# Optimization experiments

Measured on AMD Instinct MI355X. Metric: run time of the kernel, lower is better.

## Reference

```python
import jax, jax.numpy as jnp
import numpy as np

GRID = 16
K = 2
NW = (GRID - K + 1) ** 2  # 225 sliding 2x2 windows on the 16x16 grid


def _make_mask():
    idx = np.arange(GRID * GRID).reshape(GRID, GRID)
    wins = np.stack([idx[i:i + K, j:j + K].ravel()
                     for i in range(GRID - K + 1) for j in range(GRID - K + 1)])
    m = np.zeros((NW, GRID * GRID), np.float32)
    m[np.arange(NW)[:, None], wins] = 1.0
    return jnp.asarray(m)

MASK = _make_mask()          # [225, 256] window -> covered cells
MASK_COUNT = MASK.sum(0)     # windows covering each cell
BN_SCALE = np.float32(1.0 / np.sqrt(1.0 + 1e-5))  # eval BN, running mean=0 var=1


def _adapter(x, w1, w2):
    return jax.nn.relu(jax.nn.relu(x @ w1.T) @ w2.T)


def _bn(x, g, b):
    return x * (g * BN_SCALE) + b


def _head(x, w1, b1, g2, be2, w2, b2, g3, be3, w3, b3):
    x = _bn(jax.nn.relu(x @ w1.T + b1), g2, be2)
    x = _bn(jax.nn.relu(x @ w2.T + b2), g3, be3)
    return jax.nn.sigmoid(x @ w3.T + b3)[:, 0]


def setup_inputs() -> dict:
    B, L, P, D, R, S = 64, 3, 225, 640, 1800, 240
    key = jax.random.key(0)
    ks = jax.random.split(key, 16)
    n = lambda k, s, sc=1.0: jax.random.normal(k, s, jnp.float32) * sc
    te = n(ks[3], (2, D)); te = te / jnp.linalg.norm(te, axis=-1, keepdims=True)
    pr = n(ks[5], (L, R, D)); pr = pr / jnp.linalg.norm(pr, axis=-1, keepdims=True)
    w = 0.05
    return dict(
        image=n(ks[0], (B, 3, S, S)),
        image_embeds=n(ks[1], (B, D)),
        patch_embeds=n(ks[2], (L, B, P, D)),
        text_embeds=te,
        image_embeds_ref=n(ks[4], (1, D)),
        patch_embeds_ref=pr,
        a_w1=n(ks[6], (160, D), w), a_w2=n(ks[7], (D, 160), w),
        r_w1=n(ks[8], (128, D), w), r_b1=jnp.zeros((128,)),
        r_g2=jnp.ones((128,)), r_be2=jnp.zeros((128,)),
        r_w2=n(ks[9], (64, 128), w), r_b2=jnp.zeros((64,)),
        r_g3=jnp.ones((64,)), r_be3=jnp.zeros((64,)),
        r_w3=n(ks[10], (1, 64), w), r_b3=jnp.zeros((1,)),
        h_w1=n(ks[11], (128, P), w), h_b1=jnp.zeros((128,)),
        h_g2=jnp.ones((128,)), h_be2=jnp.zeros((128,)),
        h_w2=n(ks[12], (64, 128), w), h_b2=jnp.zeros((64,)),
        h_g3=jnp.ones((64,)), h_be3=jnp.zeros((64,)),
        h_w3=n(ks[13], (1, 64), w), h_b3=jnp.zeros((1,)),
    )


def reference(image, image_embeds, patch_embeds, text_embeds, image_embeds_ref,
              patch_embeds_ref, a_w1, a_w2,
              r_w1, r_b1, r_g2, r_be2, r_w2, r_b2, r_g3, r_be3, r_w3, r_b3,
              h_w1, h_b1, h_g2, h_be2, h_w2, h_b2, h_g3, h_be3, h_w3, h_b3):
    pe = patch_embeds / jnp.linalg.norm(patch_embeds, axis=-1, keepdims=True)
    nie = image_embeds / jnp.linalg.norm(image_embeds, axis=-1, keepdims=True)
    text_score = jax.nn.softmax(100.0 * nie @ text_embeds.T, axis=-1)[:, 1]
    # kNN-style min-distance over reference patches: [L,B,P,R]
    sim = jnp.einsum('lbpd,lrd->lbpr', pe, patch_embeds_ref)
    patch_ref_map = ((1.0 - sim).min(axis=3) / 2.0).mean(axis=0)  # [B,P]
    fg_score = patch_ref_map.max(axis=1)
    diff = image_embeds_ref - _adapter(image_embeds, a_w1, a_w2)
    img_ref_score = _head(diff, r_w1, r_b1, r_g2, r_be2, r_w2, r_b2, r_g3, r_be3, r_w3, r_b3)
    holistic = (text_score + img_ref_score)[:, None] + patch_ref_map  # [B,225]
    hl_score = _head(holistic, h_w1, h_b1, h_g2, h_be2, h_w2, h_b2, h_g3, h_be3, h_w3, h_b3)
    final_score = (hl_score + fg_score) / 2.0
    # harmonic aggregation of window scores onto the 16x16 grid
    heat = (MASK_COUNT / ((1.0 / holistic) @ MASK)).reshape(-1, GRID, GRID)
    hmap = jax.image.resize(heat, (heat.shape[0], image.shape[2], image.shape[3]), 'bilinear')
    return final_score, hmap
```

## Files before the change

kernel.cpp:

```cpp
#include <hip/hip_runtime.h>
#include <stdint.h>
#include <math.h>

#define L_DIM 3
#define B_DIM 64
#define P_DIM 225
#define D_DIM 640
#define R_DIM 1800
#define S_DIM 240
#define M_TOT 14400
#define M_PAD 14592
#define N_PAD 2048
#define MT 57
#define NT 8
#define KT 10
#define BNSCALE 0.99999500003749981f

typedef __bf16 bf16x8 __attribute__((ext_vector_type(8)));
typedef float f32x4 __attribute__((ext_vector_type(4)));

__device__ __forceinline__ unsigned short f2bf(float f) {
    union { float f; unsigned u; } v; v.f = f;
    unsigned u = v.u;
    unsigned r = (u + 0x7FFFu + ((u >> 16) & 1u)) >> 16;
    return (unsigned short)r;
}

__global__ __launch_bounds__(256)
void k_convert(const float* __restrict__ pe, const float* __restrict__ per,
               unsigned short* __restrict__ abf, unsigned short* __restrict__ rbf,
               float* __restrict__ rnorm)
{
    const int AROWS = L_DIM * M_PAD;
    int wid = (blockIdx.x * 256 + threadIdx.x) >> 6;
    int lane = threadIdx.x & 63;
    const ushort4 z4 = {0, 0, 0, 0};
    if (wid < AROWS) {
        int l = wid / M_PAD, r = wid - l * M_PAD;
        unsigned short* dst = abf + (size_t)wid * D_DIM;
        if (r < M_TOT) {
            const float4* src = (const float4*)(pe + ((size_t)l * M_TOT + r) * D_DIM);
            float ss = 0.f;
            #pragma unroll
            for (int it = 0; it < 3; ++it) {
                int idx = it * 64 + lane;
                if (idx < 160) {
                    float4 v = src[idx];
                    ss += v.x * v.x + v.y * v.y + v.z * v.z + v.w * v.w;
                    ushort4 o;
                    o.x = f2bf(v.x); o.y = f2bf(v.y); o.z = f2bf(v.z); o.w = f2bf(v.w);
                    *(ushort4*)(dst + idx * 4) = o;
                }
            }
            #pragma unroll
            for (int m = 32; m; m >>= 1) ss += __shfl_xor(ss, m);
            if (lane == 0) rnorm[l * M_TOT + r] = rsqrtf(ss);
        } else {
            #pragma unroll
            for (int it = 0; it < 3; ++it) {
                int idx = it * 64 + lane;
                if (idx < 160) *(ushort4*)(dst + idx * 4) = z4;
            }
        }
    } else {
        int w2 = wid - AROWS;
        int l = w2 / N_PAD, r = w2 - l * N_PAD;
        unsigned short* dst = rbf + (size_t)w2 * D_DIM;
        if (r < R_DIM) {
            const float4* src = (const float4*)(per + ((size_t)l * R_DIM + r) * D_DIM);
            #pragma unroll
            for (int it = 0; it < 3; ++it) {
                int idx = it * 64 + lane;
                if (idx < 160) {
                    float4 v = src[idx];
                    ushort4 o;
                    o.x = f2bf(v.x); o.y = f2bf(v.y); o.z = f2bf(v.z); o.w = f2bf(v.w);
                    *(ushort4*)(dst + idx * 4) = o;
                }
            }
        } else {
            #pragma unroll
            for (int it = 0; it < 3; ++it) {
                int idx = it * 64 + lane;
                if (idx < 160) *(ushort4*)(dst + idx * 4) = z4;
            }
        }
    }
}

#define MFMA(A, B, C) __builtin_amdgcn_mfma_f32_16x16x32_bf16((A), (B), (C), 0, 0, 0)
#define GLL(SRC, DSTOFF)                                                     \
    __builtin_amdgcn_global_load_lds(                                        \
        (const __attribute__((address_space(1))) void*)(SRC),               \
        (__attribute__((address_space(3))) void*)(lds + (DSTOFF)), 16, 0, 0)

#define PHASE_TAIL(NJB, STG0, STG1, VMSTR)                                   \
    {                                                                        \
        bf16x8 b00 = *(const bf16x8*)(lds + bB + (brow0 + (NJB) * 16) * 64 + sw0);     \
        bf16x8 b01 = *(const bf16x8*)(lds + bB + (brow0 + (NJB) * 16) * 64 + sw1);     \
        bf16x8 b10 = *(const bf16x8*)(lds + bB + (brow0 + (NJB + 1) * 16) * 64 + sw0); \
        bf16x8 b11 = *(const bf16x8*)(lds + bB + (brow0 + (NJB + 1) * 16) * 64 + sw1); \
        STG0; STG1;                                                          \
        asm volatile("s_waitcnt " VMSTR ::: "memory");                       \
        __builtin_amdgcn_s_barrier();                                        \
        __builtin_amdgcn_s_setprio(1);                                       \
        _Pragma("unroll")                                                    \
        for (int mi = 0; mi < 4; ++mi) {                                     \
            acc[mi][NJB]     = MFMA(a[mi][0], b00, acc[mi][NJB]);            \
            acc[mi][NJB]     = MFMA(a[mi][1], b01, acc[mi][NJB]);            \
            acc[mi][NJB + 1] = MFMA(a[mi][0], b10, acc[mi][NJB + 1]);        \
            acc[mi][NJB + 1] = MFMA(a[mi][1], b11, acc[mi][NJB + 1]);        \
        }                                                                    \
        __builtin_amdgcn_s_setprio(0);                                       \
    }

__global__ __launch_bounds__(512, 2)
void k_gemm_max(const unsigned short* __restrict__ abf,
                const unsigned short* __restrict__ rbf,
                float* __restrict__ pmax)
{
    __shared__ unsigned short lds[65536];
    __shared__ float red[2][256];

    int bid = blockIdx.x;
    int v = (bid & 7) * 171 + (bid >> 3);
    int l = v / (MT * NT);
    int rem = v - l * (MT * NT);
    int mt = rem >> 3;
    int nt = rem & 7;

    int tid = threadIdx.x;
    int wid = tid >> 6, lane = tid & 63;
    int wm = wid >> 1;
    int wn = wid & 1;
    int lane15 = lane & 15, lg = lane >> 4;
    int sA = lane15 & 7;
    int sw0 = ((lg) ^ sA) << 3;
    int sw1 = ((4 + lg) ^ sA) << 3;
    int arow0 = wm * 64 + lane15;
    int brow0 = wn * 128 + lane15;

    int rowc = lane >> 3;
    int scol = ((lane & 7) ^ rowc) << 3;
    const unsigned short* gA = abf + (size_t)(l * M_PAD + mt * 256) * D_DIM;
    const unsigned short* gB = rbf + (size_t)(l * N_PAD + nt * 256) * D_DIM;
    int chA0 = wid, chA1 = 8 + wid, chA2 = 16 + wid, chA3 = 24 + wid;
    int chB0 = (wid < 4) ? (0 + wid) : (12 + wid);
    int chB1 = (wid < 4) ? (4 + wid) : (16 + wid);
    int chB2 = (wid < 4) ? (8 + wid) : (20 + wid);
    int chB3 = (wid < 4) ? (12 + wid) : (24 + wid);
    const unsigned short* pA0 = gA + (size_t)(chA0 * 8 + rowc) * D_DIM + scol;
    const unsigned short* pA1 = gA + (size_t)(chA1 * 8 + rowc) * D_DIM + scol;
    const unsigned short* pA2 = gA + (size_t)(chA2 * 8 + rowc) * D_DIM + scol;
    const unsigned short* pA3 = gA + (size_t)(chA3 * 8 + rowc) * D_DIM + scol;
    const unsigned short* pB0 = gB + (size_t)(chB0 * 8 + rowc) * D_DIM + scol;
    const unsigned short* pB1 = gB + (size_t)(chB1 * 8 + rowc) * D_DIM + scol;
    const unsigned short* pB2 = gB + (size_t)(chB2 * 8 + rowc) * D_DIM + scol;
    const unsigned short* pB3 = gB + (size_t)(chB3 * 8 + rowc) * D_DIM + scol;

    f32x4 acc[4][8];
    #pragma unroll
    for (int mi = 0; mi < 4; ++mi)
        #pragma unroll
        for (int nj = 0; nj < 8; ++nj)
            acc[mi][nj] = f32x4{0.f, 0.f, 0.f, 0.f};

    GLL(pA0, chA0 * 512); GLL(pA1, chA1 * 512);
    GLL(pA2, chA2 * 512); GLL(pA3, chA3 * 512);
    GLL(pB0, 32768 + chB0 * 512); GLL(pB1, 32768 + chB1 * 512);
    GLL(pB2, 32768 + chB2 * 512); GLL(pB3, 32768 + chB3 * 512);
    asm volatile("s_waitcnt vmcnt(3)" ::: "memory");
    __builtin_amdgcn_s_barrier();

    int buf = 0;
    for (int kt = 0; kt < KT; ++kt) {
        int ob = buf ^ 1;
        int aB = buf * 16384;
        int bB = 32768 + buf * 16384;
        int oaB = ob * 16384;
        int obB = 32768 + ob * 16384;
        int koff = (kt + 1 < KT ? kt + 1 : KT - 1) * 64;

        bf16x8 a[4][2];
        #pragma unroll
        for (int mi = 0; mi < 4; ++mi) {
            a[mi][0] = *(const bf16x8*)(lds + aB + (arow0 + mi * 16) * 64 + sw0);
            a[mi][1] = *(const bf16x8*)(lds + aB + (arow0 + mi * 16) * 64 + sw1);
        }
        PHASE_TAIL(0, GLL(pA0 + koff, oaB + chA0 * 512),
                      GLL(pA1 + koff, oaB + chA1 * 512), "vmcnt(4)")
        PHASE_TAIL(2, GLL(pA2 + koff, oaB + chA2 * 512),
                      GLL(pA3 + koff, oaB + chA3 * 512), "vmcnt(5)")
        PHASE_TAIL(4, GLL(pB0 + koff, obB + chB0 * 512),
                      GLL(pB1 + koff, obB + chB1 * 512), "vmcnt(6)")
        PHASE_TAIL(6, GLL(pB2 + koff, obB + chB2 * 512),
                      GLL(pB3 + koff, obB + chB3 * 512), "vmcnt(3)")
        buf = ob;
    }

    __syncthreads();

    int colbase = nt * 256 + wn * 128 + lane15;
    #pragma unroll
    for (int mi = 0; mi < 4; ++mi) {
        float t[4] = {-__builtin_inff(), -__builtin_inff(),
                      -__builtin_inff(), -__builtin_inff()};
        #pragma unroll
        for (int nj = 0; nj < 8; ++nj) {
            if (colbase + nj * 16 < R_DIM) {
                #pragma unroll
                for (int r = 0; r < 4; ++r) t[r] = fmaxf(t[r], acc[mi][nj][r]);
            }
        }
        #pragma unroll
        for (int m = 1; m <= 8; m <<= 1) {
            #pragma unroll
            for (int r = 0; r < 4; ++r) t[r] = fmaxf(t[r], __shfl_xor(t[r], m));
        }
        if (lane15 == 0) {
            int rb = wm * 64 + mi * 16 + lg * 4;
            #pragma unroll
            for (int r = 0; r < 4; ++r) red[wn][rb + r] = t[r];
        }
    }
    __syncthreads();
    if (tid < 256) {
        float vmx = fmaxf(red[0][tid], red[1][tid]);
        pmax[((size_t)l * NT + nt) * M_PAD + mt * 256 + tid] = vmx;
    }
}

__global__ __launch_bounds__(256)
void k_combine(const float* __restrict__ pmax, const float* __restrict__ rnorm,
               float* __restrict__ prm)
{
    int r = blockIdx.x * 256 + threadIdx.x;
    if (r >= M_TOT) return;
    float s = 0.f;
    #pragma unroll
    for (int l = 0; l < L_DIM; ++l) {
        float m = -__builtin_inff();
        #pragma unroll
        for (int t = 0; t < NT; ++t)
            m = fmaxf(m, pmax[((size_t)l * NT + t) * M_PAD + r]);
        s += m * rnorm[l * M_TOT + r];
    }
    prm[r] = (3.0f - s) / 6.0f;
}

__device__ __forceinline__ float block_sum8(float v, volatile float* scratch) {
    #pragma unroll
    for (int m = 32; m; m >>= 1) v += __shfl_xor(v, m);
    int w = threadIdx.x >> 6;
    __syncthreads();
    if ((threadIdx.x & 63) == 0) scratch[w] = v;
    __syncthreads();
    float r = 0.f;
    #pragma unroll
    for (int i = 0; i < 8; ++i) r += scratch[i];
    return r;
}
__device__ __forceinline__ float block_max8(float v, volatile float* scratch) {
    #pragma unroll
    for (int m = 32; m; m >>= 1) v = fmaxf(v, __shfl_xor(v, m));
    int w = threadIdx.x >> 6;
    __syncthreads();
    if ((threadIdx.x & 63) == 0) scratch[w] = v;
    __syncthreads();
    float r = scratch[0];
    #pragma unroll
    for (int i = 1; i < 8; ++i) r = fmaxf(r, scratch[i]);
    return r;
}

__global__ __launch_bounds__(512)
void k_small(const float* __restrict__ ie, const float* __restrict__ te,
             const float* __restrict__ ier,
             const float* __restrict__ a_w1, const float* __restrict__ a_w2,
             const float* __restrict__ r_w1, const float* __restrict__ r_b1,
             const float* __restrict__ r_g2, const float* __restrict__ r_be2,
             const float* __restrict__ r_w2, const float* __restrict__ r_b2,
             const float* __restrict__ r_g3, const float* __restrict__ r_be3,
             const float* __restrict__ r_w3, const float* __restrict__ r_b3,
             const float* __restrict__ h_w1, const float* __restrict__ h_b1,
             const float* __restrict__ h_g2, const float* __restrict__ h_be2,
             const float* __restrict__ h_w2, const float* __restrict__ h_b2,
             const float* __restrict__ h_g3, const float* __restrict__ h_be3,
             const float* __restrict__ h_w3, const float* __restrict__ h_b3,
             const float* __restrict__ prm, float* __restrict__ heat,
             float* __restrict__ out_score)
{
    int b = blockIdx.x, tid = threadIdx.x;
    __shared__ float x[D_DIM];
    __shared__ float h1[160];
    __shared__ float dif[D_DIM];
    __shared__ float z1[128];
    __shared__ float z2[64];
    __shared__ float hol[P_DIM];
    __shared__ float rcp[P_DIM];
    __shared__ float scratch[8];

    for (int i = tid; i < D_DIM; i += 512) x[i] = ie[b * D_DIM + i];
    __syncthreads();

    float ss = 0.f, d0 = 0.f, d1 = 0.f;
    for (int i = tid; i < D_DIM; i += 512) {
        float v = x[i];
        ss += v * v;
        d0 += v * te[i];
        d1 += v * te[D_DIM + i];
    }
    float ssum = block_sum8(ss, scratch);
    float dd0 = block_sum8(d0, scratch);
    float dd1 = block_sum8(d1, scratch);
    float tscore = 1.f / (1.f + expf(100.f * rsqrtf(ssum) * (dd0 - dd1)));

    for (int o = tid; o < 160; o += 512) {
        const float* w = a_w1 + (size_t)o * D_DIM;
        float s0 = 0, s1 = 0, s2 = 0, s3 = 0;
        for (int d = 0; d < D_DIM; d += 4) {
            s0 += x[d] * w[d]; s1 += x[d + 1] * w[d + 1];
            s2 += x[d + 2] * w[d + 2]; s3 += x[d + 3] * w[d + 3];
        }
        h1[o] = fmaxf((s0 + s1) + (s2 + s3), 0.f);
    }
    __syncthreads();
    for (int d = tid; d < D_DIM; d += 512) {
        const float* w = a_w2 + (size_t)d * 160;
        float s0 = 0, s1 = 0, s2 = 0, s3 = 0;
        for (int o = 0; o < 160; o += 4) {
            s0 += h1[o] * w[o]; s1 += h1[o + 1] * w[o + 1];
            s2 += h1[o + 2] * w[o + 2]; s3 += h1[o + 3] * w[o + 3];
        }
        dif[d] = ier[d] - fmaxf((s0 + s1) + (s2 + s3), 0.f);
    }
    __syncthreads();

    for (int o = tid; o < 128; o += 512) {
        const float* w = r_w1 + (size_t)o * D_DIM;
        float s0 = 0, s1 = 0, s2 = 0, s3 = 0;
        for (int d = 0; d < D_DIM; d += 4) {
            s0 += dif[d] * w[d]; s1 += dif[d + 1] * w[d + 1];
            s2 += dif[d + 2] * w[d + 2]; s3 += dif[d + 3] * w[d + 3];
        }
        float s = (s0 + s1) + (s2 + s3) + r_b1[o];
        z1[o] = fmaxf(s, 0.f) * (r_g2[o] * BNSCALE) + r_be2[o];
    }
    __syncthreads();
    for (int o = tid; o < 64; o += 512) {
        const float* w = r_w2 + (size_t)o * 128;
        float s = r_b2[o];
        for (int d = 0; d < 128; ++d) s += z1[d] * w[d];
        z2[o] = fmaxf(s, 0.f) * (r_g3[o] * BNSCALE) + r_be3[o];
    }
    __syncthreads();
    float sp = (tid < 64) ? z2[tid] * r_w3[tid] : 0.f;
    float irs = 1.f / (1.f + expf(-(block_sum8(sp, scratch) + r_b3[0])));

    float fgp = -__builtin_inff();
    float base = tscore + irs;
    for (int p = tid; p < P_DIM; p += 512) {
        float pv = prm[b * P_DIM + p];
        fgp = fmaxf(fgp, pv);
        float h = base + pv;
        hol[p] = h;
        rcp[p] = 1.f / h;
    }
    float fg = block_max8(fgp, scratch);

    for (int o = tid; o < 128; o += 512) {
        const float* w = h_w1 + (size_t)o * P_DIM;
        float s = h_b1[o];
        for (int d = 0; d < P_DIM; ++d) s += hol[d] * w[d];
        z1[o] = fmaxf(s, 0.f) * (h_g2[o] * BNSCALE) + h_be2[o];
    }
    __syncthreads();
    for (int o = tid; o < 64; o += 512) {
        const float* w = h_w2 + (size_t)o * 128;
        float s = h_b2[o];
        for (int d = 0; d < 128; ++d) s += z1[d] * w[d];
        z2[o] = fmaxf(s, 0.f) * (h_g3[o] * BNSCALE) + h_be3[o];
    }
    __syncthreads();
    float sp2 = (tid < 64) ? z2[tid] * h_w3[tid] : 0.f;
    float hl_in = block_sum8(sp2, scratch) + h_b3[0];
    if (tid == 0) {
        float hl = 1.f / (1.f + expf(-hl_in));
        out_score[b] = (hl + fg) * 0.5f;
    }

    if (tid < 256) {
        int r = tid >> 4, c = tid & 15;
        float s = 0.f, cnt = 0.f;
        #pragma unroll
        for (int di = -1; di <= 0; ++di) {
            int i = r + di;
            if (i < 0 || i > 14) continue;
            #pragma unroll
            for (int dj = -1; dj <= 0; ++dj) {
                int j = c + dj;
                if (j < 0 || j > 14) continue;
                s += rcp[i * 15 + j];
                cnt += 1.f;
            }
        }
        heat[b * 256 + tid] = cnt / s;
    }
}

__global__ __launch_bounds__(256)
void k_resize(const float* __restrict__ heat, float* __restrict__ outh)
{
    int b = blockIdx.x >> 3, sub = blockIdx.x & 7;
    __shared__ float h[256];
    if (threadIdx.x < 256) h[threadIdx.x] = heat[b * 256 + threadIdx.x];
    __syncthreads();
    int base = sub * 30 * S_DIM;
    for (int q = threadIdx.x; q < 30 * S_DIM; q += 256) {
        int px = base + q;
        int y = px / S_DIM, xc = px - y * S_DIM;
        float sy = fminf(fmaxf((y - 7) * (1.0f / 15.0f), 0.f), 15.f);
        float sx = fminf(fmaxf((xc - 7) * (1.0f / 15.0f), 0.f), 15.f);
        int y0 = (int)sy, x0 = (int)sx;
        int y1 = min(y0 + 1, 15), x1 = min(x0 + 1, 15);
        float fy = sy - (float)y0, fx = sx - (float)x0;
        float v00 = h[y0 * 16 + x0], v01 = h[y0 * 16 + x1];
        float v10 = h[y1 * 16 + x0], v11 = h[y1 * 16 + x1];
        float v = (1.f - fy) * ((1.f - fx) * v00 + fx * v01)
                + fy * ((1.f - fx) * v10 + fx * v11);
        outh[(size_t)b * (S_DIM * S_DIM) + px] = v;
    }
}

extern "C" void kernel_launch(void* const* d_in, const int* in_sizes, int n_in,
                              void* d_out, int out_size, void* d_ws, size_t ws_size,
                              hipStream_t stream)
{
    (void)in_sizes; (void)n_in; (void)out_size; (void)ws_size;
    const float* image_embeds = (const float*)d_in[1];
    const float* patch_embeds = (const float*)d_in[2];
    const float* text_embeds  = (const float*)d_in[3];
    const float* ier          = (const float*)d_in[4];
    const float* per          = (const float*)d_in[5];
    const float* a_w1 = (const float*)d_in[6];
    const float* a_w2 = (const float*)d_in[7];
    const float* r_w1 = (const float*)d_in[8];
    const float* r_b1 = (const float*)d_in[9];
    const float* r_g2 = (const float*)d_in[10];
    const float* r_be2 = (const float*)d_in[11];
    const float* r_w2 = (const float*)d_in[12];
    const float* r_b2 = (const float*)d_in[13];
    const float* r_g3 = (const float*)d_in[14];
    const float* r_be3 = (const float*)d_in[15];
    const float* r_w3 = (const float*)d_in[16];
    const float* r_b3 = (const float*)d_in[17];
    const float* h_w1 = (const float*)d_in[18];
    const float* h_b1 = (const float*)d_in[19];
    const float* h_g2 = (const float*)d_in[20];
    const float* h_be2 = (const float*)d_in[21];
    const float* h_w2 = (const float*)d_in[22];
    const float* h_b2 = (const float*)d_in[23];
    const float* h_g3 = (const float*)d_in[24];
    const float* h_be3 = (const float*)d_in[25];
    const float* h_w3 = (const float*)d_in[26];
    const float* h_b3 = (const float*)d_in[27];

    char* ws = (char*)d_ws;
    size_t off = 0;
    auto take = [&](size_t bytes) -> void* {
        void* p = ws + off;
        off += (bytes + 255) & ~(size_t)255;
        return p;
    };
    float* rnorm = (float*)take((size_t)L_DIM * M_TOT * 4);
    float* pmax  = (float*)take((size_t)L_DIM * NT * M_PAD * 4);
    float* prm   = (float*)take((size_t)M_TOT * 4);
    float* heat  = (float*)take((size_t)B_DIM * 256 * 4);
    unsigned short* abf = (unsigned short*)take((size_t)L_DIM * M_PAD * D_DIM * 2);
    unsigned short* rbf = (unsigned short*)take((size_t)L_DIM * N_PAD * D_DIM * 2);

    float* out_f = (float*)d_out;

    k_convert<<<dim3((L_DIM * M_PAD + L_DIM * N_PAD) / 4), dim3(256), 0, stream>>>(
        patch_embeds, per, abf, rbf, rnorm);
    k_gemm_max<<<dim3(L_DIM * MT * NT), dim3(512), 0, stream>>>(abf, rbf, pmax);
    k_combine<<<dim3((M_TOT + 255) / 256), dim3(256), 0, stream>>>(pmax, rnorm, prm);
    k_small<<<dim3(B_DIM), dim3(512), 0, stream>>>(image_embeds, text_embeds, ier,
        a_w1, a_w2, r_w1, r_b1, r_g2, r_be2, r_w2, r_b2, r_g3, r_be3, r_w3, r_b3,
        h_w1, h_b1, h_g2, h_be2, h_w2, h_b2, h_g3, h_be3, h_w3, h_b3,
        prm, heat, out_f);
    k_resize<<<dim3(B_DIM * 8), dim3(256), 0, stream>>>(heat, out_f + B_DIM);
}
```

Measured before the change: 204.5 us.

## Software-pipeline LDS fragment reads in GEMM and fuse combine into small kernel

The GEMM inner loop now prefetches the next B-quarter and the next k-tile's A/B fragments into registers before issuing the current MFMAs, ping-ponging between two register sets. The goal is to hide LDS read latency behind MFMA work instead of stalling after each barrier. The separate k_combine kernel is removed and its max/normalize reduction is folded into k_small, which saves one launch and a round trip through global memory. In exchange the prefetch buffers raise register pressure at launch_bounds(512,2), and k_small's per-block work grows slightly.

```diff
diff --git a/kernel.cpp b/kernel.cpp
--- a/kernel.cpp
+++ b/kernel.cpp
@@ -94,25 +94,26 @@
         (const __attribute__((address_space(1))) void*)(SRC),               \
         (__attribute__((address_space(3))) void*)(lds + (DSTOFF)), 16, 0, 0)
 
-#define PHASE_TAIL(NJB, STG0, STG1, VMSTR)                                   \
-    {                                                                        \
-        bf16x8 b00 = *(const bf16x8*)(lds + bB + (brow0 + (NJB) * 16) * 64 + sw0);     \
-        bf16x8 b01 = *(const bf16x8*)(lds + bB + (brow0 + (NJB) * 16) * 64 + sw1);     \
-        bf16x8 b10 = *(const bf16x8*)(lds + bB + (brow0 + (NJB + 1) * 16) * 64 + sw0); \
-        bf16x8 b11 = *(const bf16x8*)(lds + bB + (brow0 + (NJB + 1) * 16) * 64 + sw1); \
-        STG0; STG1;                                                          \
-        asm volatile("s_waitcnt " VMSTR ::: "memory");                       \
-        __builtin_amdgcn_s_barrier();                                        \
-        __builtin_amdgcn_s_setprio(1);                                       \
-        _Pragma("unroll")                                                    \
-        for (int mi = 0; mi < 4; ++mi) {                                     \
-            acc[mi][NJB]     = MFMA(a[mi][0], b00, acc[mi][NJB]);            \
-            acc[mi][NJB]     = MFMA(a[mi][1], b01, acc[mi][NJB]);            \
-            acc[mi][NJB + 1] = MFMA(a[mi][0], b10, acc[mi][NJB + 1]);        \
-            acc[mi][NJB + 1] = MFMA(a[mi][1], b11, acc[mi][NJB + 1]);        \
-        }                                                                    \
-        __builtin_amdgcn_s_setprio(0);                                       \
-    }
+#define RD_BQ(D0, D1, D2, D3, Q, BASE) do {                                  \
+    D0 = *(const bf16x8*)(lds + (BASE) + (brow0 + (Q) * 32) * 64 + sw0);     \
+    D1 = *(const bf16x8*)(lds + (BASE) + (brow0 + (Q) * 32) * 64 + sw1);     \
+    D2 = *(const bf16x8*)(lds + (BASE) + (brow0 + (Q) * 32 + 16) * 64 + sw0);\
+    D3 = *(const bf16x8*)(lds + (BASE) + (brow0 + (Q) * 32 + 16) * 64 + sw1);\
+} while (0)
+
+#define RD_A(BASE) do { _Pragma("unroll")                                    \
+    for (int mi = 0; mi < 4; ++mi) {                                         \
+        a[mi][0] = *(const bf16x8*)(lds + (BASE) + (arow0 + mi * 16) * 64 + sw0); \
+        a[mi][1] = *(const bf16x8*)(lds + (BASE) + (arow0 + mi * 16) * 64 + sw1); \
+    } } while (0)
+
+#define MM(NJB, B0, B1, B2, B3) do { _Pragma("unroll")                       \
+    for (int mi = 0; mi < 4; ++mi) {                                         \
+        acc[mi][NJB]     = MFMA(a[mi][0], B0, acc[mi][NJB]);                 \
+        acc[mi][NJB]     = MFMA(a[mi][1], B1, acc[mi][NJB]);                 \
+        acc[mi][NJB + 1] = MFMA(a[mi][0], B2, acc[mi][NJB + 1]);             \
+        acc[mi][NJB + 1] = MFMA(a[mi][1], B3, acc[mi][NJB + 1]);             \
+    } } while (0)
 
 __global__ __launch_bounds__(512, 2)
 void k_gemm_max(const unsigned short* __restrict__ abf,
@@ -172,29 +173,52 @@
     asm volatile("s_waitcnt vmcnt(3)" ::: "memory");
     __builtin_amdgcn_s_barrier();
 
+    bf16x8 a[4][2];
+    bf16x8 ba0, ba1, ba2, ba3, bb0, bb1, bb2, bb3;
+    RD_A(0);
+    RD_BQ(ba0, ba1, ba2, ba3, 0, 32768);
+
     int buf = 0;
     for (int kt = 0; kt < KT; ++kt) {
         int ob = buf ^ 1;
-        int aB = buf * 16384;
         int bB = 32768 + buf * 16384;
         int oaB = ob * 16384;
         int obB = 32768 + ob * 16384;
         int koff = (kt + 1 < KT ? kt + 1 : KT - 1) * 64;
 
-        bf16x8 a[4][2];
-        #pragma unroll
-        for (int mi = 0; mi < 4; ++mi) {
-            a[mi][0] = *(const bf16x8*)(lds + aB + (arow0 + mi * 16) * 64 + sw0);
-            a[mi][1] = *(const bf16x8*)(lds + aB + (arow0 + mi * 16) * 64 + sw1);
-        }
-        PHASE_TAIL(0, GLL(pA0 + koff, oaB + chA0 * 512),
-                      GLL(pA1 + koff, oaB + chA1 * 512), "vmcnt(4)")
-        PHASE_TAIL(2, GLL(pA2 + koff, oaB + chA2 * 512),
-                      GLL(pA3 + koff, oaB + chA3 * 512), "vmcnt(5)")
-        PHASE_TAIL(4, GLL(pB0 + koff, obB + chB0 * 512),
-                      GLL(pB1 + koff, obB + chB1 * 512), "vmcnt(6)")
-        PHASE_TAIL(6, GLL(pB2 + koff, obB + chB2 * 512),
-                      GLL(pB3 + koff, obB + chB3 * 512), "vmcnt(3)")
+        GLL(pA0 + koff, oaB + chA0 * 512); GLL(pA1 + koff, oaB + chA1 * 512);
+        asm volatile("s_waitcnt vmcnt(4)" ::: "memory");
+        __builtin_amdgcn_s_barrier();
+        RD_BQ(bb0, bb1, bb2, bb3, 1, bB);
+        __builtin_amdgcn_s_setprio(1);
+        MM(0, ba0, ba1, ba2, ba3);
+        __builtin_amdgcn_s_setprio(0);
+
+        GLL(pA2 + koff, oaB + chA2 * 512); GLL(pA3 + koff, oaB + chA3 * 512);
+        asm volatile("s_waitcnt vmcnt(5)" ::: "memory");
+        __builtin_amdgcn_s_barrier();
+        RD_BQ(ba0, ba1, ba2, ba3, 2, bB);
+        __builtin_amdgcn_s_setprio(1);
+        MM(2, bb0, bb1, bb2, bb3);
+        __builtin_amdgcn_s_setprio(0);
+
+        GLL(pB0 + koff, obB + chB0 * 512); GLL(pB1 + koff, obB + chB1 * 512);
+        asm volatile("s_waitcnt vmcnt(6)" ::: "memory");
+        __builtin_amdgcn_s_barrier();
+        RD_BQ(bb0, bb1, bb2, bb3, 3, bB);
+        __builtin_amdgcn_s_setprio(1);
+        MM(4, ba0, ba1, ba2, ba3);
+        __builtin_amdgcn_s_setprio(0);
+
+        GLL(pB2 + koff, obB + chB2 * 512); GLL(pB3 + koff, obB + chB3 * 512);
+        asm volatile("s_waitcnt vmcnt(3)" ::: "memory");
+        __builtin_amdgcn_s_barrier();
+        RD_A(oaB);
+        RD_BQ(ba0, ba1, ba2, ba3, 0, obB);
+        __builtin_amdgcn_s_setprio(1);
+        MM(6, bb0, bb1, bb2, bb3);
+        __builtin_amdgcn_s_setprio(0);
+
         buf = ob;
     }
 
@@ -228,24 +252,6 @@
         float vmx = fmaxf(red[0][tid], red[1][tid]);
         pmax[((size_t)l * NT + nt) * M_PAD + mt * 256 + tid] = vmx;
     }
-}
-
-__global__ __launch_bounds__(256)
-void k_combine(const float* __restrict__ pmax, const float* __restrict__ rnorm,
-               float* __restrict__ prm)
-{
-    int r = blockIdx.x * 256 + threadIdx.x;
-    if (r >= M_TOT) return;
-    float s = 0.f;
-    #pragma unroll
-    for (int l = 0; l < L_DIM; ++l) {
-        float m = -__builtin_inff();
-        #pragma unroll
-        for (int t = 0; t < NT; ++t)
-            m = fmaxf(m, pmax[((size_t)l * NT + t) * M_PAD + r]);
-        s += m * rnorm[l * M_TOT + r];
-    }
-    prm[r] = (3.0f - s) / 6.0f;
 }
 
 __device__ __forceinline__ float block_sum8(float v, volatile float* scratch) {
@@ -287,8 +293,8 @@
              const float* __restrict__ h_w2, const float* __restrict__ h_b2,
              const float* __restrict__ h_g3, const float* __restrict__ h_be3,
              const float* __restrict__ h_w3, const float* __restrict__ h_b3,
-             const float* __restrict__ prm, float* __restrict__ heat,
-             float* __restrict__ out_score)
+             const float* __restrict__ pmax, const float* __restrict__ rnorm,
+             float* __restrict__ heat, float* __restrict__ out_score)
 {
     int b = blockIdx.x, tid = threadIdx.x;
     __shared__ float x[D_DIM];
@@ -360,7 +366,17 @@
     float fgp = -__builtin_inff();
     float base = tscore + irs;
     for (int p = tid; p < P_DIM; p += 512) {
-        float pv = prm[b * P_DIM + p];
+        int r = b * P_DIM + p;
+        float s = 0.f;
+        #pragma unroll
+        for (int l = 0; l < L_DIM; ++l) {
+            float m = -__builtin_inff();
+            #pragma unroll
+            for (int t = 0; t < NT; ++t)
+                m = fmaxf(m, pmax[((size_t)l * NT + t) * M_PAD + r]);
+            s += m * rnorm[l * M_TOT + r];
+        }
+        float pv = (3.0f - s) / 6.0f;
         fgp = fmaxf(fgp, pv);
         float h = base + pv;
         hol[p] = h;
@@ -474,7 +490,6 @@
     };
     float* rnorm = (float*)take((size_t)L_DIM * M_TOT * 4);
     float* pmax  = (float*)take((size_t)L_DIM * NT * M_PAD * 4);
-    float* prm   = (float*)take((size_t)M_TOT * 4);
     float* heat  = (float*)take((size_t)B_DIM * 256 * 4);
     unsigned short* abf = (unsigned short*)take((size_t)L_DIM * M_PAD * D_DIM * 2);
     unsigned short* rbf = (unsigned short*)take((size_t)L_DIM * N_PAD * D_DIM * 2);
@@ -484,10 +499,9 @@
     k_convert<<<dim3((L_DIM * M_PAD + L_DIM * N_PAD) / 4), dim3(256), 0, stream>>>(
         patch_embeds, per, abf, rbf, rnorm);
     k_gemm_max<<<dim3(L_DIM * MT * NT), dim3(512), 0, stream>>>(abf, rbf, pmax);
-    k_combine<<<dim3((M_TOT + 255) / 256), dim3(256), 0, stream>>>(pmax, rnorm, prm);
     k_small<<<dim3(B_DIM), dim3(512), 0, stream>>>(image_embeds, text_embeds, ier,
         a_w1, a_w2, r_w1, r_b1, r_g2, r_be2, r_w2, r_b2, r_g3, r_be3, r_w3, r_b3,
         h_w1, h_b1, h_g2, h_be2, h_w2, h_b2, h_g3, h_be3, h_w3, h_b3,
-        prm, heat, out_f);
+        pmax, rnorm, heat, out_f);
     k_resize<<<dim3(B_DIM * 8), dim3(256), 0, stream>>>(heat, out_f + B_DIM);
 }
```

Result: slower. 212.4 us (+3.8%).
